# Optimization experiments

Hardware: AMD Instinct MI355X
Metric: run time of the kernel (lower is better)

The kernel has to match this reference:

```python
import jax, jax.numpy as jnp
import numpy as np

D_MODEL, D_CTX, D_HEAD = 1024, 768, 16

def setup_inputs() -> dict:
    key = jax.random.key(0)
    ks = jax.random.split(key, 10)
    B, M, N = 8, 4096, 4096
    s = lambda d: 1.0 / np.sqrt(d)
    return {
        "x": jax.random.normal(ks[0], (B, M, D_MODEL), dtype=jnp.float32),
        "context": jax.random.normal(ks[1], (B, N, D_CTX), dtype=jnp.float32),
        "Wq": jax.random.uniform(ks[2], (D_MODEL, D_HEAD), jnp.float32, -s(D_MODEL), s(D_MODEL)),
        "bq": jax.random.uniform(ks[3], (D_HEAD,), jnp.float32, -s(D_MODEL), s(D_MODEL)),
        "Wk": jax.random.uniform(ks[4], (D_CTX, D_HEAD), jnp.float32, -s(D_CTX), s(D_CTX)),
        "bk": jax.random.uniform(ks[5], (D_HEAD,), jnp.float32, -s(D_CTX), s(D_CTX)),
        "Wv": jax.random.uniform(ks[6], (D_CTX, D_HEAD), jnp.float32, -s(D_CTX), s(D_CTX)),
        "bv": jax.random.uniform(ks[7], (D_HEAD,), jnp.float32, -s(D_CTX), s(D_CTX)),
        "Wo": jax.random.uniform(ks[8], (D_HEAD, D_MODEL), jnp.float32, -s(D_HEAD), s(D_HEAD)),
        "bo": jax.random.uniform(ks[9], (D_MODEL,), jnp.float32, -s(D_HEAD), s(D_HEAD)),
    }

def _kernel(t):
    # ELU+1 feature map (non-negative)
    return jax.nn.elu(t) + 1.0

def reference(x, context, Wq, bq, Wk, bk, Wv, bv, Wo, bo):
    Q = _kernel(x @ Wq + bq)            # (B, M, d_head)
    K = _kernel(context @ Wk + bk)      # (B, N, d_head)
    V = context @ Wv + bv               # (B, N, d_head)
    KtV = jnp.einsum('bnd,bne->bde', K, V)   # (B, d_head, d_head)
    num = jnp.einsum('bmd,bde->bme', Q, KtV) # (B, M, d_head)
    K_sum = K.sum(axis=1)                    # (B, d_head)
    denom = jnp.einsum('bmd,bd->bm', Q, K_sum)[..., None] + 1e-6
    out = num / denom                        # (B, M, d_head)
    return out @ Wo + bo                     # (B, M, d_model)
```

## Files before the change

kernel.cpp:

```cpp
#include <hip/hip_runtime.h>
#include <math.h>

#define B_   8
#define M_   4096
#define N_   4096
#define DM   1024
#define DC   768
#define DH   16
#define PD   8
#define KVBLOCKS (B_*N_/32)
#define QBLOCKS  (B_*M_/32)
#define CHUNKS   128

typedef float v4f __attribute__((ext_vector_type(4)));
typedef __attribute__((ext_vector_type(8))) short short8v;
typedef __attribute__((ext_vector_type(4))) float f32x4;
typedef __attribute__((ext_vector_type(4))) int int4v;

__device__ __forceinline__ float elu1(float t) {
    return t > 0.0f ? t + 1.0f : expf(t);
}
__device__ __forceinline__ float4 ld4(const float* p) { return *reinterpret_cast<const float4*>(p); }
__device__ __forceinline__ void  st4(float* p, float4 v) { *reinterpret_cast<float4*>(p) = v; }
__device__ __forceinline__ void  st4nt(float* p, float4 v) {
    v4f w; w.x = v.x; w.y = v.y; w.z = v.z; w.w = v.w;
    __builtin_nontemporal_store(w, reinterpret_cast<v4f*>(p));
}
__device__ __forceinline__ void fma4(float4& a, float s, float4 w) {
    a.x = fmaf(s, w.x, a.x); a.y = fmaf(s, w.y, a.y);
    a.z = fmaf(s, w.z, a.z); a.w = fmaf(s, w.w, a.w);
}
__device__ __forceinline__ short f2bf(float f) {
    unsigned u = __float_as_uint(f);
    unsigned r = 0x7FFFu + ((u >> 16) & 1u);
    return (short)((u + r) >> 16);
}
__device__ __forceinline__ unsigned cvtpk(float a, float b) {
    unsigned r;
    asm("v_cvt_pk_bf16_f32 %0, %1, %2" : "=v"(r) : "v"(a), "v"(b));
    return r;
}
__device__ __forceinline__ short8v mk_frag(const float4& a, const float4& b) {
    int4v iv;
    iv.x = (int)cvtpk(a.x, a.y);
    iv.y = (int)cvtpk(a.z, a.w);
    iv.z = (int)cvtpk(b.x, b.y);
    iv.w = (int)cvtpk(b.z, b.w);
    union { int4v i; short8v s; } u; u.i = iv;
    return u.s;
}

__global__ __launch_bounds__(256) void prep(
    const float* __restrict__ Wq, const float* __restrict__ Wk,
    const float* __restrict__ Wv,
    short* __restrict__ fq, short* __restrict__ fk, short* __restrict__ fv)
{
    const int id = blockIdx.x * 256 + threadIdx.x;
    if (id >= 80 * 64) return;
    const int l  = id & 63;
    const int kt = id >> 6;
    const float* W; short* dst; int ktl;
    if (kt < 32)      { W = Wq; dst = fq; ktl = kt; }
    else if (kt < 56) { W = Wk; dst = fk; ktl = kt - 32; }
    else              { W = Wv; dst = fv; ktl = kt - 56; }
    const int k0 = ktl * 32 + (l >> 4) * 8;
    const int d  = l & 15;
    short* o = dst + ((size_t)ktl * 64 + l) * 8;
    #pragma unroll
    for (int j = 0; j < 8; ++j)
        o[j] = f2bf(W[(size_t)(k0 + j) * DH + d]);
}

__global__ __launch_bounds__(256) void fused1(
    const float* __restrict__ ctx, const float* __restrict__ x,
    const short* __restrict__ fq, const short* __restrict__ fk,
    const short* __restrict__ fv,
    const float* __restrict__ bq, const float* __restrict__ bk,
    const float* __restrict__ bv,
    float* __restrict__ part, float* __restrict__ q_ws)
{
    __shared__ union {
        struct {
            float ka[2][2][16][17];
            float va[2][2][16][17];
            float sk[32][17];
            float sv[32][17];
        } kv;
        struct {
            float qa[2][2][16][17];
        } q;
    } sh;

    const int t  = threadIdx.x;
    const int l  = t & 63;
    const int w  = t >> 6;
    const int rt = w & 1;
    const int kh = w >> 1;
    const int g4 = l >> 4;
    const int lr = l & 15;

    float4 pa[PD], pb[PD];

    if (blockIdx.x < KVBLOCKS) {
        const size_t row0 = (size_t)blockIdx.x * 32;
        const float* src = ctx + (row0 + rt*16 + lr) * DC + kh*384 + g4*8;
        f32x4 accK = {0,0,0,0}, accV = {0,0,0,0};

        #pragma unroll
        for (int i = 0; i < PD; ++i) {
            pa[i] = ld4(src + i*32);
            pb[i] = ld4(src + i*32 + 4);
        }
        #pragma unroll
        for (int kt = 0; kt < 12; ++kt) {
            const int st = kt & (PD-1);
            const short8v a = mk_frag(pa[st], pb[st]);
            if (kt + PD < 12) {
                pa[st] = ld4(src + (kt+PD)*32);
                pb[st] = ld4(src + (kt+PD)*32 + 4);
            }
            const int ktg = kh*12 + kt;
            const short8v bkf = *reinterpret_cast<const short8v*>(fk + ((size_t)ktg*64 + l)*8);
            const short8v bvf = *reinterpret_cast<const short8v*>(fv + ((size_t)ktg*64 + l)*8);
            accK = __builtin_amdgcn_mfma_f32_16x16x32_bf16(a, bkf, accK, 0, 0, 0);
            accV = __builtin_amdgcn_mfma_f32_16x16x32_bf16(a, bvf, accV, 0, 0, 0);
        }

        #pragma unroll
        for (int j = 0; j < 4; ++j) {
            sh.kv.ka[rt][kh][g4*4 + j][lr] = accK[j];
            sh.kv.va[rt][kh][g4*4 + j][lr] = accV[j];
        }
        __syncthreads();

        #pragma unroll
        for (int i = t; i < 512; i += 256) {
            const int r = i >> 4, c = i & 15;
            const int rr = r >> 4, wr = r & 15;
            const float kk = sh.kv.ka[rr][0][wr][c] + sh.kv.ka[rr][1][wr][c] + bk[c];
            const float vv = sh.kv.va[rr][0][wr][c] + sh.kv.va[rr][1][wr][c] + bv[c];
            sh.kv.sk[r][c] = elu1(kk);
            sh.kv.sv[r][c] = vv;
        }
        __syncthreads();

        const int d = t >> 4, e = t & 15;
        float acc = 0.f;
        #pragma unroll 16
        for (int n = 0; n < 32; ++n) acc += sh.kv.sk[n][d] * sh.kv.sv[n][e];
        float* p = part + (size_t)blockIdx.x * 272;
        p[t] = acc;
        if (t < DH) {
            float ss = 0.f;
            #pragma unroll 16
            for (int n = 0; n < 32; ++n) ss += sh.kv.sk[n][t];
            p[256 + t] = ss;
        }
    } else {
        const size_t row0 = (size_t)(blockIdx.x - KVBLOCKS) * 32;
        const float* src = x + (row0 + rt*16 + lr) * DM + kh*512 + g4*8;
        f32x4 accQ = {0,0,0,0};

        #pragma unroll
        for (int i = 0; i < PD; ++i) {
            pa[i] = ld4(src + i*32);
            pb[i] = ld4(src + i*32 + 4);
        }
        #pragma unroll
        for (int kt = 0; kt < 16; ++kt) {
            const int st = kt & (PD-1);
            const short8v a = mk_frag(pa[st], pb[st]);
            if (kt + PD < 16) {
                pa[st] = ld4(src + (kt+PD)*32);
                pb[st] = ld4(src + (kt+PD)*32 + 4);
            }
            const int ktg = kh*16 + kt;
            const short8v bqf = *reinterpret_cast<const short8v*>(fq + ((size_t)ktg*64 + l)*8);
            accQ = __builtin_amdgcn_mfma_f32_16x16x32_bf16(a, bqf, accQ, 0, 0, 0);
        }

        #pragma unroll
        for (int j = 0; j < 4; ++j)
            sh.q.qa[rt][kh][g4*4 + j][lr] = accQ[j];
        __syncthreads();

        #pragma unroll
        for (int i = t; i < 512; i += 256) {
            const int r = i >> 4, c = i & 15;
            const int rr = r >> 4, wr = r & 15;
            const float v = sh.q.qa[rr][0][wr][c] + sh.q.qa[rr][1][wr][c] + bq[c];
            q_ws[(row0 + r)*DH + c] = elu1(v);
        }
    }
}

__global__ __launch_bounds__(320) void reduce2(
    const float* __restrict__ part, float* __restrict__ comb)
{
    const int b = blockIdx.x;
    const int t = threadIdx.x;
    if (t < 272) {
        float s = 0.f;
        #pragma unroll
        for (int ch = 0; ch < CHUNKS; ++ch)
            s += part[((size_t)b*CHUNKS + ch) * 272 + t];
        comb[(size_t)b*272 + t] = s;
    }
}

__global__ __launch_bounds__(256) void oproj(
    const float* __restrict__ q_ws, const float* __restrict__ comb,
    const float* __restrict__ Wo, const float* __restrict__ bo,
    float* __restrict__ out)
{
    __shared__ float ql[16 * DH];
    __shared__ float ol[16 * DH];
    __shared__ float kts[272];

    const int t = threadIdx.x;
    const size_t row0 = (size_t)blockIdx.x * 16;
    const int b = blockIdx.x >> 8;

    float4 wreg[16];
    #pragma unroll
    for (int e = 0; e < 16; ++e) wreg[e] = ld4(Wo + (size_t)e*DM + t*4);
    const float4 bov = ld4(bo + t*4);

    if (t < 64) st4(&ql[t*4], ld4(q_ws + row0*DH + t*4));
    else if (t < 132) st4(&kts[(t-64)*4], ld4(comb + (size_t)b*272 + (t-64)*4));
    __syncthreads();

    if (t < 64) {
        const float* qrow = &ql[(t >> 2) * DH];
        const int jj = (t & 3) * 4;
        float den = 1e-6f;
        float4 num = make_float4(0,0,0,0);
        #pragma unroll
        for (int d4 = 0; d4 < 4; ++d4) {
            const float4 q4  = ld4(&qrow[d4*4]);
            const float4 ks4 = ld4(&kts[256 + d4*4]);
            den += q4.x*ks4.x + q4.y*ks4.y + q4.z*ks4.z + q4.w*ks4.w;
            fma4(num, q4.x, ld4(&kts[(d4*4+0)*DH + jj]));
            fma4(num, q4.y, ld4(&kts[(d4*4+1)*DH + jj]));
            fma4(num, q4.z, ld4(&kts[(d4*4+2)*DH + jj]));
            fma4(num, q4.w, ld4(&kts[(d4*4+3)*DH + jj]));
        }
        const float inv = 1.0f / den;
        float4 o4; o4.x = num.x*inv; o4.y = num.y*inv; o4.z = num.z*inv; o4.w = num.w*inv;
        st4(&ol[(t >> 2)*DH + jj], o4);
    }
    __syncthreads();

    #pragma unroll
    for (int r = 0; r < 16; ++r) {
        float4 a = bov;
        #pragma unroll
        for (int eo = 0; eo < 4; ++eo) {
            const float4 o4 = ld4(&ol[r*DH + eo*4]);
            fma4(a, o4.x, wreg[eo*4+0]); fma4(a, o4.y, wreg[eo*4+1]);
            fma4(a, o4.z, wreg[eo*4+2]); fma4(a, o4.w, wreg[eo*4+3]);
        }
        st4nt(out + (row0 + r)*DM + t*4, a);
    }
}

extern "C" void kernel_launch(void* const* d_in, const int* in_sizes, int n_in,
                              void* d_out, int out_size, void* d_ws, size_t ws_size,
                              hipStream_t stream) {
    const float* x    = (const float*)d_in[0];
    const float* ctx  = (const float*)d_in[1];
    const float* Wq   = (const float*)d_in[2];
    const float* bq   = (const float*)d_in[3];
    const float* Wk   = (const float*)d_in[4];
    const float* bk   = (const float*)d_in[5];
    const float* Wv   = (const float*)d_in[6];
    const float* bv   = (const float*)d_in[7];
    const float* Wo   = (const float*)d_in[8];
    const float* bo   = (const float*)d_in[9];
    float* out = (float*)d_out;

    float* ws = (float*)d_ws;
    float* part = ws;
    float* comb = part + (size_t)KVBLOCKS*272;
    float* q_ws = comb + (size_t)B_*272;
    short* fq = (short*)(q_ws + (size_t)B_*M_*DH);
    short* fk = fq + (size_t)32*64*8;
    short* fv = fk + (size_t)24*64*8;

    prep<<<dim3(20), dim3(256), 0, stream>>>(Wq, Wk, Wv, fq, fk, fv);
    fused1<<<dim3(KVBLOCKS + QBLOCKS), dim3(256), 0, stream>>>(
        ctx, x, fq, fk, fv, bq, bk, bv, part, q_ws);
    reduce2<<<dim3(B_), dim3(320), 0, stream>>>(part, comb);
    oproj<<<dim3(B_*M_/16), dim3(256), 0, stream>>>(q_ws, comb, Wo, bo, out);
}
```

Before: 81.29 us.

## Fuse Q projection into output-projection kernel, drop Q workspace round trip

Moves the Q projection (x@Wq, bias, ELU+1) out of the first fused kernel and into the output-projection kernel. Each 16-row block now computes its own Q tile with MFMA, keeps it in shared memory and immediately applies KtV, normalisation and Wo. This removes the q_ws global write and reread. It also makes the first kernel a KV-only pass, at the cost of the x reads now running after the KV reduction instead of overlapping with the ctx reads. The Wo register load is moved after the Q stage to limit register pressure.

```diff
diff --git a/kernel.cpp b/kernel.cpp
--- a/kernel.cpp
+++ b/kernel.cpp
@@ -9,7 +9,6 @@
 #define DH   16
 #define PD   8
 #define KVBLOCKS (B_*N_/32)
-#define QBLOCKS  (B_*M_/32)
 #define CHUNKS   128
 
 typedef float v4f __attribute__((ext_vector_type(4)));
@@ -71,24 +70,17 @@
         o[j] = f2bf(W[(size_t)(k0 + j) * DH + d]);
 }
 
-__global__ __launch_bounds__(256) void fused1(
-    const float* __restrict__ ctx, const float* __restrict__ x,
-    const short* __restrict__ fq, const short* __restrict__ fk,
-    const short* __restrict__ fv,
-    const float* __restrict__ bq, const float* __restrict__ bk,
-    const float* __restrict__ bv,
-    float* __restrict__ part, float* __restrict__ q_ws)
-{
-    __shared__ union {
-        struct {
-            float ka[2][2][16][17];
-            float va[2][2][16][17];
-            float sk[32][17];
-            float sv[32][17];
-        } kv;
-        struct {
-            float qa[2][2][16][17];
-        } q;
+__global__ __launch_bounds__(256) void kvr(
+    const float* __restrict__ ctx,
+    const short* __restrict__ fk, const short* __restrict__ fv,
+    const float* __restrict__ bk, const float* __restrict__ bv,
+    float* __restrict__ part)
+{
+    __shared__ struct {
+        float ka[2][2][16][17];
+        float va[2][2][16][17];
+        float sk[32][17];
+        float sv[32][17];
     } sh;
 
     const int t  = threadIdx.x;
@@ -100,97 +92,59 @@
     const int lr = l & 15;
 
     float4 pa[PD], pb[PD];
-
-    if (blockIdx.x < KVBLOCKS) {
-        const size_t row0 = (size_t)blockIdx.x * 32;
-        const float* src = ctx + (row0 + rt*16 + lr) * DC + kh*384 + g4*8;
-        f32x4 accK = {0,0,0,0}, accV = {0,0,0,0};
-
-        #pragma unroll
-        for (int i = 0; i < PD; ++i) {
-            pa[i] = ld4(src + i*32);
-            pb[i] = ld4(src + i*32 + 4);
+    const size_t row0 = (size_t)blockIdx.x * 32;
+    const float* src = ctx + (row0 + rt*16 + lr) * DC + kh*384 + g4*8;
+    f32x4 accK = {0,0,0,0}, accV = {0,0,0,0};
+
+    #pragma unroll
+    for (int i = 0; i < PD; ++i) {
+        pa[i] = ld4(src + i*32);
+        pb[i] = ld4(src + i*32 + 4);
+    }
+    #pragma unroll
+    for (int kt = 0; kt < 12; ++kt) {
+        const int st = kt & (PD-1);
+        const short8v a = mk_frag(pa[st], pb[st]);
+        if (kt + PD < 12) {
+            pa[st] = ld4(src + (kt+PD)*32);
+            pb[st] = ld4(src + (kt+PD)*32 + 4);
         }
-        #pragma unroll
-        for (int kt = 0; kt < 12; ++kt) {
-            const int st = kt & (PD-1);
-            const short8v a = mk_frag(pa[st], pb[st]);
-            if (kt + PD < 12) {
-                pa[st] = ld4(src + (kt+PD)*32);
-                pb[st] = ld4(src + (kt+PD)*32 + 4);
-            }
-            const int ktg = kh*12 + kt;
-            const short8v bkf = *reinterpret_cast<const short8v*>(fk + ((size_t)ktg*64 + l)*8);
-            const short8v bvf = *reinterpret_cast<const short8v*>(fv + ((size_t)ktg*64 + l)*8);
-            accK = __builtin_amdgcn_mfma_f32_16x16x32_bf16(a, bkf, accK, 0, 0, 0);
-            accV = __builtin_amdgcn_mfma_f32_16x16x32_bf16(a, bvf, accV, 0, 0, 0);
-        }
-
-        #pragma unroll
-        for (int j = 0; j < 4; ++j) {
-            sh.kv.ka[rt][kh][g4*4 + j][lr] = accK[j];
-            sh.kv.va[rt][kh][g4*4 + j][lr] = accV[j];
-        }
-        __syncthreads();
-
-        #pragma unroll
-        for (int i = t; i < 512; i += 256) {
-            const int r = i >> 4, c = i & 15;
-            const int rr = r >> 4, wr = r & 15;
-            const float kk = sh.kv.ka[rr][0][wr][c] + sh.kv.ka[rr][1][wr][c] + bk[c];
-            const float vv = sh.kv.va[rr][0][wr][c] + sh.kv.va[rr][1][wr][c] + bv[c];
-            sh.kv.sk[r][c] = elu1(kk);
-            sh.kv.sv[r][c] = vv;
-        }
-        __syncthreads();
-
-        const int d = t >> 4, e = t & 15;
-        float acc = 0.f;
+        const int ktg = kh*12 + kt;
+        const short8v bkf = *reinterpret_cast<const short8v*>(fk + ((size_t)ktg*64 + l)*8);
+        const short8v bvf = *reinterpret_cast<const short8v*>(fv + ((size_t)ktg*64 + l)*8);
+        accK = __builtin_amdgcn_mfma_f32_16x16x32_bf16(a, bkf, accK, 0, 0, 0);
+        accV = __builtin_amdgcn_mfma_f32_16x16x32_bf16(a, bvf, accV, 0, 0, 0);
+    }
+
+    #pragma unroll
+    for (int j = 0; j < 4; ++j) {
+        sh.ka[rt][kh][g4*4 + j][lr] = accK[j];
+        sh.va[rt][kh][g4*4 + j][lr] = accV[j];
+    }
+    __syncthreads();
+
+    #pragma unroll
+    for (int i = t; i < 512; i += 256) {
+        const int r = i >> 4, c = i & 15;
+        const int rr = r >> 4, wr = r & 15;
+        const float kk = sh.ka[rr][0][wr][c] + sh.ka[rr][1][wr][c] + bk[c];
+        const float vv = sh.va[rr][0][wr][c] + sh.va[rr][1][wr][c] + bv[c];
+        sh.sk[r][c] = elu1(kk);
+        sh.sv[r][c] = vv;
+    }
+    __syncthreads();
+
+    const int d = t >> 4, e = t & 15;
+    float acc = 0.f;
+    #pragma unroll 16
+    for (int n = 0; n < 32; ++n) acc += sh.sk[n][d] * sh.sv[n][e];
+    float* p = part + (size_t)blockIdx.x * 272;
+    p[t] = acc;
+    if (t < DH) {
+        float ss = 0.f;
         #pragma unroll 16
-        for (int n = 0; n < 32; ++n) acc += sh.kv.sk[n][d] * sh.kv.sv[n][e];
-        float* p = part + (size_t)blockIdx.x * 272;
-        p[t] = acc;
-        if (t < DH) {
-            float ss = 0.f;
-            #pragma unroll 16
-            for (int n = 0; n < 32; ++n) ss += sh.kv.sk[n][t];
-            p[256 + t] = ss;
-        }
-    } else {
-        const size_t row0 = (size_t)(blockIdx.x - KVBLOCKS) * 32;
-        const float* src = x + (row0 + rt*16 + lr) * DM + kh*512 + g4*8;
-        f32x4 accQ = {0,0,0,0};
-
-        #pragma unroll
-        for (int i = 0; i < PD; ++i) {
-            pa[i] = ld4(src + i*32);
-            pb[i] = ld4(src + i*32 + 4);
-        }
-        #pragma unroll
-        for (int kt = 0; kt < 16; ++kt) {
-            const int st = kt & (PD-1);
-            const short8v a = mk_frag(pa[st], pb[st]);
-            if (kt + PD < 16) {
-                pa[st] = ld4(src + (kt+PD)*32);
-                pb[st] = ld4(src + (kt+PD)*32 + 4);
-            }
-            const int ktg = kh*16 + kt;
-            const short8v bqf = *reinterpret_cast<const short8v*>(fq + ((size_t)ktg*64 + l)*8);
-            accQ = __builtin_amdgcn_mfma_f32_16x16x32_bf16(a, bqf, accQ, 0, 0, 0);
-        }
-
-        #pragma unroll
-        for (int j = 0; j < 4; ++j)
-            sh.q.qa[rt][kh][g4*4 + j][lr] = accQ[j];
-        __syncthreads();
-
-        #pragma unroll
-        for (int i = t; i < 512; i += 256) {
-            const int r = i >> 4, c = i & 15;
-            const int rr = r >> 4, wr = r & 15;
-            const float v = sh.q.qa[rr][0][wr][c] + sh.q.qa[rr][1][wr][c] + bq[c];
-            q_ws[(row0 + r)*DH + c] = elu1(v);
-        }
+        for (int n = 0; n < 32; ++n) ss += sh.sk[n][t];
+        p[256 + t] = ss;
     }
 }
 
@@ -208,26 +162,52 @@
     }
 }
 
-__global__ __launch_bounds__(256) void oproj(
-    const float* __restrict__ q_ws, const float* __restrict__ comb,
+__global__ __launch_bounds__(256) void qproj(
+    const float* __restrict__ x,
+    const short* __restrict__ fq, const float* __restrict__ bq,
+    const float* __restrict__ comb,
     const float* __restrict__ Wo, const float* __restrict__ bo,
     float* __restrict__ out)
 {
+    __shared__ float qa[4][16][17];
     __shared__ float ql[16 * DH];
     __shared__ float ol[16 * DH];
     __shared__ float kts[272];
 
-    const int t = threadIdx.x;
+    const int t  = threadIdx.x;
+    const int l  = t & 63;
+    const int w  = t >> 6;
+    const int g4 = l >> 4;
+    const int lr = l & 15;
     const size_t row0 = (size_t)blockIdx.x * 16;
     const int b = blockIdx.x >> 8;
 
-    float4 wreg[16];
-    #pragma unroll
-    for (int e = 0; e < 16; ++e) wreg[e] = ld4(Wo + (size_t)e*DM + t*4);
-    const float4 bov = ld4(bo + t*4);
-
-    if (t < 64) st4(&ql[t*4], ld4(q_ws + row0*DH + t*4));
-    else if (t < 132) st4(&kts[(t-64)*4], ld4(comb + (size_t)b*272 + (t-64)*4));
+    const float* src = x + (row0 + lr) * DM + w*256 + g4*8;
+    float4 pa[8], pb[8];
+    #pragma unroll
+    for (int i = 0; i < 8; ++i) {
+        pa[i] = ld4(src + i*32);
+        pb[i] = ld4(src + i*32 + 4);
+    }
+    if (t < 68) st4(&kts[t*4], ld4(comb + (size_t)b*272 + t*4));
+
+    f32x4 accQ = {0,0,0,0};
+    #pragma unroll
+    for (int kt = 0; kt < 8; ++kt) {
+        const short8v a = mk_frag(pa[kt], pb[kt]);
+        const short8v bqf = *reinterpret_cast<const short8v*>(fq + ((size_t)(w*8 + kt)*64 + l)*8);
+        accQ = __builtin_amdgcn_mfma_f32_16x16x32_bf16(a, bqf, accQ, 0, 0, 0);
+    }
+    #pragma unroll
+    for (int j = 0; j < 4; ++j)
+        qa[w][g4*4 + j][lr] = accQ[j];
+    __syncthreads();
+
+    {
+        const int r = t >> 4, c = t & 15;
+        const float v = qa[0][r][c] + qa[1][r][c] + qa[2][r][c] + qa[3][r][c] + bq[c];
+        ql[r*DH + c] = elu1(v);
+    }
     __syncthreads();
 
     if (t < 64) {
@@ -251,6 +231,11 @@
     }
     __syncthreads();
 
+    float4 wreg[16];
+    #pragma unroll
+    for (int e = 0; e < 16; ++e) wreg[e] = ld4(Wo + (size_t)e*DM + t*4);
+    const float4 bov = ld4(bo + t*4);
+
     #pragma unroll
     for (int r = 0; r < 16; ++r) {
         float4 a = bov;
@@ -282,14 +267,12 @@
     float* ws = (float*)d_ws;
     float* part = ws;
     float* comb = part + (size_t)KVBLOCKS*272;
-    float* q_ws = comb + (size_t)B_*272;
-    short* fq = (short*)(q_ws + (size_t)B_*M_*DH);
+    short* fq = (short*)(comb + (size_t)B_*272);
     short* fk = fq + (size_t)32*64*8;
     short* fv = fk + (size_t)24*64*8;
 
     prep<<<dim3(20), dim3(256), 0, stream>>>(Wq, Wk, Wv, fq, fk, fv);
-    fused1<<<dim3(KVBLOCKS + QBLOCKS), dim3(256), 0, stream>>>(
-        ctx, x, fq, fk, fv, bq, bk, bv, part, q_ws);
+    kvr<<<dim3(KVBLOCKS), dim3(256), 0, stream>>>(ctx, fk, fv, bk, bv, part);
     reduce2<<<dim3(B_), dim3(320), 0, stream>>>(part, comb);
-    oproj<<<dim3(B_*M_/16), dim3(256), 0, stream>>>(q_ws, comb, Wo, bo, out);
-}
+    qproj<<<dim3(B_*M_/16), dim3(256), 0, stream>>>(x, fq, bq, comb, Wo, bo, out);
+}
```

Measured after the change: 73.49 us. 9.6% less time.
